# Kernel tuning notes

Hardware: AMD Instinct MI355X
Metric: run time of the kernel (lower is better)

## Reference

```python
import jax, jax.numpy as jnp
import numpy as np

B, L, S = 4, 1024, 1024
D_MODEL, H, DK = 1024, 16, 64  # d_model == H * DK required by the in-place writeback


def setup_inputs() -> dict:
    key = jax.random.key(0)
    ks = jax.random.split(key, 12)
    queries = jax.random.normal(ks[0], (B, L, D_MODEL), dtype=jnp.float32)
    keys = jax.random.normal(ks[1], (B, S, D_MODEL), dtype=jnp.float32)
    values = jax.random.normal(ks[2], (B, S, D_MODEL), dtype=jnp.float32)
    gate_scores = jax.random.uniform(ks[3], (B, H, DK, D_MODEL), dtype=jnp.float32)
    sc = 1.0 / np.sqrt(D_MODEL)
    W_q = jax.random.normal(ks[4], (H * DK, D_MODEL), dtype=jnp.float32) * sc
    b_q = jax.random.normal(ks[5], (H * DK,), dtype=jnp.float32) * 0.01
    W_k = jax.random.normal(ks[6], (H * DK, D_MODEL), dtype=jnp.float32) * sc
    b_k = jax.random.normal(ks[7], (H * DK,), dtype=jnp.float32) * 0.01
    W_v = jax.random.normal(ks[8], (H * DK, D_MODEL), dtype=jnp.float32) * sc
    b_v = jax.random.normal(ks[9], (H * DK,), dtype=jnp.float32) * 0.01
    W_o = jax.random.normal(ks[10], (D_MODEL, H * DK), dtype=jnp.float32) * sc
    b_o = jax.random.normal(ks[11], (D_MODEL,), dtype=jnp.float32) * 0.01
    return {"queries": queries, "keys": keys, "values": values,
            "gate_scores": gate_scores, "W_q": W_q, "b_q": b_q,
            "W_k": W_k, "b_k": b_k, "W_v": W_v, "b_v": b_v,
            "W_o": W_o, "b_o": b_o}


def reference(queries, keys, values, gate_scores, W_q, b_q, W_k, b_k, W_v, b_v, W_o, b_o):
    # Per-sample gated Q/K/V projection: W_x[b] = gate_scores[b] * W_x  (elementwise, [H,DK,Dm])
    # fused as a batched einsum instead of the per-sample Python loop.
    Wq = W_q.reshape(H, DK, D_MODEL)
    Wk = W_k.reshape(H, DK, D_MODEL)
    Wv = W_v.reshape(H, DK, D_MODEL)
    Q = jnp.einsum('blm,bhkm,hkm->blhk', queries, gate_scores, Wq) + b_q.reshape(H, DK)
    K = jnp.einsum('bsm,bhkm,hkm->bshk', keys, gate_scores, Wk) + b_k.reshape(H, DK)
    V = jnp.einsum('bsm,bhkm,hkm->bshk', values, gate_scores, Wv) + b_v.reshape(H, DK)
    # Full scaled dot-product attention (standard inner_attention)
    scale = 1.0 / jnp.sqrt(jnp.asarray(DK, Q.dtype))
    scores = jnp.einsum('blhk,bshk->bhls', Q, K) * scale
    attn = jax.nn.softmax(scores, axis=-1)
    out = jnp.einsum('bhls,bshk->blhk', attn, V).reshape(B, L, H * DK)
    out = out @ W_o.T + b_o
    return out, attn
```

## Files before the change

kernel.cpp:

```cpp
#include <hip/hip_runtime.h>
#include <math.h>

#define BB 4
#define LL 1024
#define SS 1024
#define DM 1024
#define HH 16
#define DKH 64
#define NH 1024
#define SM_SCALE 0.125f

typedef __attribute__((ext_vector_type(8))) short bf16x8;
typedef __attribute__((ext_vector_type(4))) float f32x4;
typedef unsigned short ushort_t;
typedef unsigned int uint_t;

#define MFMA16(a, b, c) __builtin_amdgcn_mfma_f32_16x16x32_bf16((a), (b), (c), 0, 0, 0)

__device__ __forceinline__ ushort_t f2b(float f) {
    union { float f; uint_t u; } x; x.f = f;
    uint_t r = x.u + 0x7fffu + ((x.u >> 16) & 1u);
    return (ushort_t)(r >> 16);
}

__device__ __forceinline__ float b2f(ushort_t v) {
    union { float f; uint_t u; } x; x.u = ((uint_t)v) << 16;
    return x.f;
}

__device__ __forceinline__ void gload_lds16(const void* g, void* l) {
    __builtin_amdgcn_global_load_lds(
        (const __attribute__((address_space(1))) unsigned int*)g,
        (__attribute__((address_space(3))) unsigned int*)l, 16, 0, 0);
}

__device__ __forceinline__ int xcd_swz(int lin, int nwg) {
    return (lin & 7) * (nwg >> 3) + (lin >> 3);
}

__device__ __forceinline__ void cvt8(const float* src, ushort_t* dst, const float* g2) {
    float4 a  = *(const float4*)(src);
    float4 b4 = *(const float4*)(src + 4);
    if (g2) {
        float4 ga = *(const float4*)(g2);
        float4 gb = *(const float4*)(g2 + 4);
        a.x *= ga.x; a.y *= ga.y; a.z *= ga.z; a.w *= ga.w;
        b4.x *= gb.x; b4.y *= gb.y; b4.z *= gb.z; b4.w *= gb.w;
    }
    uint4 o;
    o.x = f2b(a.x)  | ((uint_t)f2b(a.y)  << 16);
    o.y = f2b(a.z)  | ((uint_t)f2b(a.w)  << 16);
    o.z = f2b(b4.x) | ((uint_t)f2b(b4.y) << 16);
    o.w = f2b(b4.z) | ((uint_t)f2b(b4.w) << 16);
    *(uint4*)dst = o;
}

__global__ __launch_bounds__(256) void prep_kernel(
    const float* __restrict__ q, const float* __restrict__ k, const float* __restrict__ v,
    const float* __restrict__ gate,
    const float* __restrict__ Wq, const float* __restrict__ Wk, const float* __restrict__ Wv,
    const float* __restrict__ Wo,
    ushort_t* __restrict__ Xq, ushort_t* __restrict__ Xk, ushort_t* __restrict__ Xv,
    ushort_t* __restrict__ Gq, ushort_t* __restrict__ Gk, ushort_t* __restrict__ Gv,
    ushort_t* __restrict__ Wo2)
{
    const int XCH = 3 * 524288;
    const int GCH = 524288;
    const int WCH = 131072;
    for (int c = blockIdx.x * 256 + threadIdx.x; c < XCH + GCH + WCH; c += gridDim.x * 256) {
        if (c < XCH) {
            int r = c >> 19;
            int e = (c & 524287) * 8;
            cvt8((r == 0 ? q : r == 1 ? k : v) + e,
                 (r == 0 ? Xq : r == 1 ? Xk : Xv) + e, nullptr);
        } else if (c < XCH + GCH) {
            int e = (c - XCH) * 8;
            int nm = e & 1048575;
            const float* g2 = gate + e;
            cvt8(Wq + nm, Gq + e, g2);
            cvt8(Wk + nm, Gk + e, g2);
            cvt8(Wv + nm, Gv + e, g2);
        } else {
            int e = (c - XCH - GCH) * 8;
            cvt8(Wo + e, Wo2 + e, nullptr);
        }
    }
}

__global__ __launch_bounds__(256) void qkv_gemm(
    const ushort_t* __restrict__ Xq, const ushort_t* __restrict__ Gq, const float* __restrict__ bq,
    const ushort_t* __restrict__ Xk, const ushort_t* __restrict__ Gk, const float* __restrict__ bk,
    const ushort_t* __restrict__ Xv, const ushort_t* __restrict__ Gv, const float* __restrict__ bv,
    ushort_t* __restrict__ Qb, ushort_t* __restrict__ Kb, ushort_t* __restrict__ Vt,
    int mode)
{
    __shared__ ushort_t As[128 * 64];
    __shared__ ushort_t Bs[128 * 64];
    const int p  = xcd_swz(blockIdx.x, gridDim.x);
    const int g2 = p >> 6;
    const int r  = p & 63;
    int b, g;
    if (mode == 0)      { b = g2 / 3;  g = g2 % 3; }
    else if (mode == 1) { b = g2 >> 1; g = g2 & 1; }
    else                { b = g2;      g = 2;      }
    const size_t off = (size_t)b * 1048576;
    const ushort_t *A, *B; const float* bias; ushort_t* C; bool brow;
    if (g == 0)      { A = Xq + off; B = Gq + off; bias = bq; C = Qb + off; brow = false; }
    else if (g == 1) { A = Xk + off; B = Gk + off; bias = bk; C = Kb + off; brow = false; }
    else             { A = Gv + off; B = Xv + off; bias = bv; C = Vt + off; brow = true;  }

    const int bm = (r >> 3) * 128;
    const int bn = (r & 7) * 128;
    const int tid = threadIdx.x;
    const int lane = tid & 63;
    const int w = tid >> 6;
    const int wr = w >> 1, wc = w & 1;
    const int lr = lane & 15, lk = lane >> 4;

    f32x4 acc[4][4];
    #pragma unroll
    for (int i = 0; i < 4; ++i)
        #pragma unroll
        for (int j = 0; j < 4; ++j)
            acc[i][j] = (f32x4){0.f, 0.f, 0.f, 0.f};

    for (int k0 = 0; k0 < 1024; k0 += 64) {
        #pragma unroll
        for (int pp = 0; pp < 4; ++pp) {
            int f = pp * 256 + tid;
            int row = f >> 3, seg = f & 7;
            int kb2 = (seg * 8) ^ ((row & 7) * 8);
            gload_lds16(A + (size_t)(bm + row) * 1024 + k0 + kb2,
                        (char*)As + ((pp * 256 + (w << 6)) << 4));
            gload_lds16(B + (size_t)(bn + row) * 1024 + k0 + kb2,
                        (char*)Bs + ((pp * 256 + (w << 6)) << 4));
        }
        __syncthreads();
        #pragma unroll
        for (int kk = 0; kk < 2; ++kk) {
            bf16x8 af[4], bfr[4];
            #pragma unroll
            for (int i = 0; i < 4; ++i) {
                int row = wr * 64 + i * 16 + lr;
                af[i] = *(const bf16x8*)&As[row * 64 + ((lk * 8 + kk * 32) ^ ((row & 7) * 8))];
            }
            #pragma unroll
            for (int j = 0; j < 4; ++j) {
                int row = wc * 64 + j * 16 + lr;
                bfr[j] = *(const bf16x8*)&Bs[row * 64 + ((lk * 8 + kk * 32) ^ ((row & 7) * 8))];
            }
            #pragma unroll
            for (int i = 0; i < 4; ++i)
                #pragma unroll
                for (int j = 0; j < 4; ++j)
                    acc[i][j] = MFMA16(af[i], bfr[j], acc[i][j]);
        }
        __syncthreads();
    }

    #pragma unroll
    for (int i = 0; i < 4; ++i)
        #pragma unroll
        for (int j = 0; j < 4; ++j)
            #pragma unroll
            for (int rr = 0; rr < 4; ++rr) {
                int row = bm + wr * 64 + i * 16 + lk * 4 + rr;
                int col = bn + wc * 64 + j * 16 + lr;
                float vv = acc[i][j][rr] + bias[brow ? row : col];
                C[(size_t)row * 1024 + col] = f2b(vv);
            }
}

__global__ __launch_bounds__(256) void fused_attn_kernel(
    const ushort_t* __restrict__ Q, const ushort_t* __restrict__ Kmat,
    const ushort_t* __restrict__ Vt, float* __restrict__ attn,
    ushort_t* __restrict__ ctx)
{
    __shared__ ushort_t Ks[2][64 * 64];
    __shared__ ushort_t Vs[2][64 * 64];
    __shared__ ushort_t Ps[64 * 64];
    const int p  = xcd_swz(blockIdx.x, gridDim.x);
    const int bh = p >> 4;
    const int b  = bh >> 4;
    const int h  = bh & 15;
    const int r0 = (p & 15) * 64;
    const int tid = threadIdx.x, lane = tid & 63, w = tid >> 6;
    const int lr = lane & 15, lk = lane >> 4;

    bf16x8 aq[2];
    {
        const ushort_t* Qrow = Q + ((size_t)b * LL + r0 + w * 16 + lr) * NH + h * DKH;
        aq[0] = *(const bf16x8*)(Qrow + lk * 8);
        aq[1] = *(const bf16x8*)(Qrow + lk * 8 + 32);
    }
    const ushort_t* Kp = Kmat + (size_t)b * SS * NH + h * DKH;
    const ushort_t* Vp = Vt + ((size_t)b * NH + h * DKH) * SS;
    ushort_t* Psw = Ps + w * 1024;

    const int srow = tid >> 3;
    const int sseg = tid & 7;
    const int skb  = (sseg * 8) ^ ((srow & 7) * 8);
    const int skb1 = (sseg * 8) ^ (((srow + 32) & 7) * 8);

#define STAGE_K(t, buf)                                                          \
    do {                                                                         \
        gload_lds16(Kp + (size_t)((t) * 64 + srow) * NH + skb,                   \
                    (char*)(&Ks[buf][0]) + ((0 * 256 + (w << 6)) << 4));         \
        gload_lds16(Kp + (size_t)((t) * 64 + srow + 32) * NH + skb1,             \
                    (char*)(&Ks[buf][0]) + ((1 * 256 + (w << 6)) << 4));         \
    } while (0)
#define STAGE_V(t, buf)                                                          \
    do {                                                                         \
        gload_lds16(Vp + (size_t)srow * SS + (t) * 64 + skb,                     \
                    (char*)(&Vs[buf][0]) + ((0 * 256 + (w << 6)) << 4));         \
        gload_lds16(Vp + (size_t)(srow + 32) * SS + (t) * 64 + skb1,             \
                    (char*)(&Vs[buf][0]) + ((1 * 256 + (w << 6)) << 4));         \
    } while (0)

    float inv[4] = {0.f, 0.f, 0.f, 0.f};

    STAGE_K(0, 0);
    __syncthreads();
    for (int t = 0; t < 16; ++t) {
        const int cur = t & 1;
        if (t < 15) STAGE_K(t + 1, cur ^ 1);
        f32x4 acc[4];
        #pragma unroll
        for (int j = 0; j < 4; ++j) acc[j] = (f32x4){0.f, 0.f, 0.f, 0.f};
        #pragma unroll
        for (int kk = 0; kk < 2; ++kk)
            #pragma unroll
            for (int j = 0; j < 4; ++j) {
                int row = j * 16 + lr;
                bf16x8 bk2 = *(const bf16x8*)&Ks[cur][row * 64 + ((lk * 8 + kk * 32) ^ ((row & 7) * 8))];
                acc[j] = MFMA16(aq[kk], bk2, acc[j]);
            }
        #pragma unroll
        for (int rr = 0; rr < 4; ++rr)
            inv[rr] += __expf(SM_SCALE * acc[0][rr]) + __expf(SM_SCALE * acc[1][rr])
                     + __expf(SM_SCALE * acc[2][rr]) + __expf(SM_SCALE * acc[3][rr]);
        __syncthreads();
    }
    #pragma unroll
    for (int rr = 0; rr < 4; ++rr) {
        float s = inv[rr];
        s += __shfl_xor(s, 1);
        s += __shfl_xor(s, 2);
        s += __shfl_xor(s, 4);
        s += __shfl_xor(s, 8);
        inv[rr] = 1.0f / s;
    }

    f32x4 occ[4];
    #pragma unroll
    for (int j = 0; j < 4; ++j) occ[j] = (f32x4){0.f, 0.f, 0.f, 0.f};
    float* Ob = attn + (((size_t)b * HH + h) * LL + r0 + w * 16) * SS;
    const int erow = lane >> 3;
    const int eseg = lane & 7;

    STAGE_K(0, 0);
    STAGE_V(0, 0);
    __syncthreads();
    for (int t = 0; t < 16; ++t) {
        const int cur = t & 1;
        if (t < 15) { STAGE_K(t + 1, cur ^ 1); STAGE_V(t + 1, cur ^ 1); }
        f32x4 acc[4];
        #pragma unroll
        for (int j = 0; j < 4; ++j) acc[j] = (f32x4){0.f, 0.f, 0.f, 0.f};
        #pragma unroll
        for (int kk = 0; kk < 2; ++kk)
            #pragma unroll
            for (int j = 0; j < 4; ++j) {
                int row = j * 16 + lr;
                bf16x8 bk2 = *(const bf16x8*)&Ks[cur][row * 64 + ((lk * 8 + kk * 32) ^ ((row & 7) * 8))];
                acc[j] = MFMA16(aq[kk], bk2, acc[j]);
            }
        #pragma unroll
        for (int j = 0; j < 4; ++j)
            #pragma unroll
            for (int rr = 0; rr < 4; ++rr) {
                int ql = lk * 4 + rr;
                float pv = __expf(SM_SCALE * acc[j][rr]) * inv[rr];
                Psw[ql * 64 + ((j * 16 + lr) ^ ((ql & 7) * 8))] = f2b(pv);
            }
        #pragma unroll
        for (int kk = 0; kk < 2; ++kk) {
            bf16x8 pa = *(const bf16x8*)&Psw[lr * 64 + ((kk * 32 + lk * 8) ^ ((lr & 7) * 8))];
            #pragma unroll
            for (int j = 0; j < 4; ++j) {
                int row = j * 16 + lr;
                bf16x8 bv2 = *(const bf16x8*)&Vs[cur][row * 64 + ((kk * 32 + lk * 8) ^ ((row & 7) * 8))];
                occ[j] = MFMA16(pa, bv2, occ[j]);
            }
        }
        float* Obt = Ob + t * 64;
        #pragma unroll
        for (int hh = 0; hh < 2; ++hh) {
            int rl = erow + hh * 8;
            bf16x8 p8 = *(const bf16x8*)&Psw[rl * 64 + ((eseg * 8) ^ ((rl & 7) * 8))];
            float4 o0 = make_float4(b2f((ushort_t)p8[0]), b2f((ushort_t)p8[1]),
                                    b2f((ushort_t)p8[2]), b2f((ushort_t)p8[3]));
            float4 o1 = make_float4(b2f((ushort_t)p8[4]), b2f((ushort_t)p8[5]),
                                    b2f((ushort_t)p8[6]), b2f((ushort_t)p8[7]));
            *(float4*)(Obt + (size_t)rl * SS + eseg * 8) = o0;
            *(float4*)(Obt + (size_t)rl * SS + eseg * 8 + 4) = o1;
        }
        __syncthreads();
    }

    #pragma unroll
    for (int j = 0; j < 4; ++j)
        #pragma unroll
        for (int rr = 0; rr < 4; ++rr)
            ctx[((size_t)b * LL + r0 + w * 16 + lk * 4 + rr) * NH + h * DKH + j * 16 + lr]
                = f2b(occ[j][rr]);
#undef STAGE_K
#undef STAGE_V
}

__global__ __launch_bounds__(256) void out_gemm(
    const ushort_t* __restrict__ A, const ushort_t* __restrict__ B,
    const float* __restrict__ bias, float* __restrict__ C)
{
    __shared__ ushort_t As[128 * 64];
    __shared__ ushort_t Bs[64 * 64];
    const int p  = xcd_swz(blockIdx.x, gridDim.x);
    const int bm = (p >> 4) * 128;
    const int bn = (p & 15) * 64;
    const int tid = threadIdx.x;
    const int lane = tid & 63;
    const int w = tid >> 6;
    const int wr = w >> 1, wc = w & 1;
    const int lr = lane & 15, lk = lane >> 4;

    f32x4 acc[4][2];
    #pragma unroll
    for (int i = 0; i < 4; ++i)
        #pragma unroll
        for (int j = 0; j < 2; ++j)
            acc[i][j] = (f32x4){0.f, 0.f, 0.f, 0.f};

    for (int k0 = 0; k0 < 1024; k0 += 64) {
        #pragma unroll
        for (int pp = 0; pp < 4; ++pp) {
            int f = pp * 256 + tid;
            int row = f >> 3, seg = f & 7;
            int kb2 = (seg * 8) ^ ((row & 7) * 8);
            gload_lds16(A + (size_t)(bm + row) * 1024 + k0 + kb2,
                        (char*)As + ((pp * 256 + (w << 6)) << 4));
        }
        #pragma unroll
        for (int pp = 0; pp < 2; ++pp) {
            int f = pp * 256 + tid;
            int row = f >> 3, seg = f & 7;
            int kb2 = (seg * 8) ^ ((row & 7) * 8);
            gload_lds16(B + (size_t)(bn + row) * 1024 + k0 + kb2,
                        (char*)Bs + ((pp * 256 + (w << 6)) << 4));
        }
        __syncthreads();
        #pragma unroll
        for (int kk = 0; kk < 2; ++kk) {
            bf16x8 af[4], bfr[2];
            #pragma unroll
            for (int i = 0; i < 4; ++i) {
                int row = wr * 64 + i * 16 + lr;
                af[i] = *(const bf16x8*)&As[row * 64 + ((lk * 8 + kk * 32) ^ ((row & 7) * 8))];
            }
            #pragma unroll
            for (int j = 0; j < 2; ++j) {
                int row = wc * 32 + j * 16 + lr;
                bfr[j] = *(const bf16x8*)&Bs[row * 64 + ((lk * 8 + kk * 32) ^ ((row & 7) * 8))];
            }
            #pragma unroll
            for (int i = 0; i < 4; ++i)
                #pragma unroll
                for (int j = 0; j < 2; ++j)
                    acc[i][j] = MFMA16(af[i], bfr[j], acc[i][j]);
        }
        __syncthreads();
    }

    #pragma unroll
    for (int i = 0; i < 4; ++i)
        #pragma unroll
        for (int j = 0; j < 2; ++j)
            #pragma unroll
            for (int rr = 0; rr < 4; ++rr) {
                int row = bm + wr * 64 + i * 16 + lk * 4 + rr;
                int col = bn + wc * 32 + j * 16 + lr;
                C[(size_t)row * DM + col] = acc[i][j][rr] + bias[col];
            }
}

extern "C" void kernel_launch(void* const* d_in, const int* in_sizes, int n_in,
                              void* d_out, int out_size, void* d_ws, size_t ws_size,
                              hipStream_t stream)
{
    const float* queries = (const float*)d_in[0];
    const float* keys    = (const float*)d_in[1];
    const float* values  = (const float*)d_in[2];
    const float* gate    = (const float*)d_in[3];
    const float* W_q     = (const float*)d_in[4];
    const float* b_q     = (const float*)d_in[5];
    const float* W_k     = (const float*)d_in[6];
    const float* b_k     = (const float*)d_in[7];
    const float* W_v     = (const float*)d_in[8];
    const float* b_v     = (const float*)d_in[9];
    const float* W_o     = (const float*)d_in[10];
    const float* b_o     = (const float*)d_in[11];

    float* out  = (float*)d_out;
    float* attn = out + (size_t)BB * LL * DM;

    char* ws = (char*)d_ws;
    const size_t U = (size_t)8 << 20;
    ushort_t* Xq = (ushort_t*)(ws);
    ushort_t* Xk = (ushort_t*)(ws + 1 * U);
    ushort_t* Xv = (ushort_t*)(ws + 2 * U);
    ushort_t* Gq = (ushort_t*)(ws + 3 * U);
    ushort_t* Gk = (ushort_t*)(ws + 4 * U);
    ushort_t* Gv = (ushort_t*)(ws + 5 * U);
    ushort_t* Vt = (ushort_t*)(ws + 6 * U);
    const bool big = ws_size >= 9 * U + ((size_t)2 << 20);
    ushort_t *Qb, *Kb, *Wo2;
    if (big) { Qb = (ushort_t*)(ws + 7 * U); Kb = (ushort_t*)(ws + 8 * U); Wo2 = (ushort_t*)(ws + 9 * U); }
    else     { Qb = Xv; Kb = Gv; Wo2 = (ushort_t*)(ws + 7 * U); }
    ushort_t* ctx = Xq;

    dim3 blk(256, 1, 1);
    prep_kernel<<<2048, blk, 0, stream>>>(queries, keys, values, gate,
                                          W_q, W_k, W_v, W_o,
                                          Xq, Xk, Xv, Gq, Gk, Gv, Wo2);
    if (big) {
        qkv_gemm<<<768, blk, 0, stream>>>(Xq, Gq, b_q, Xk, Gk, b_k,
                                          Xv, Gv, b_v, Qb, Kb, Vt, 0);
    } else {
        qkv_gemm<<<256, blk, 0, stream>>>(Xq, Gq, b_q, Xk, Gk, b_k,
                                          Xv, Gv, b_v, Qb, Kb, Vt, 2);
        qkv_gemm<<<512, blk, 0, stream>>>(Xq, Gq, b_q, Xk, Gk, b_k,
                                          Xv, Gv, b_v, Qb, Kb, Vt, 1);
    }
    fused_attn_kernel<<<1024, blk, 0, stream>>>(Qb, Kb, Vt, attn, ctx);
    out_gemm<<<512, blk, 0, stream>>>(ctx, Wo2, b_o, out);
}
```

Measured before the change: 178.2 us.

## Cache unnormalized exp scores in registers to skip second QK^T pass

```diff
diff --git a/kernel.cpp b/kernel.cpp
--- a/kernel.cpp
+++ b/kernel.cpp
@@ -171,13 +171,12 @@
             }
 }
 
-__global__ __launch_bounds__(256) void fused_attn_kernel(
+__global__ __launch_bounds__(256, 2) void fused_attn_kernel(
     const ushort_t* __restrict__ Q, const ushort_t* __restrict__ Kmat,
     const ushort_t* __restrict__ Vt, float* __restrict__ attn,
     ushort_t* __restrict__ ctx)
 {
-    __shared__ ushort_t Ks[2][64 * 64];
-    __shared__ ushort_t Vs[2][64 * 64];
+    __shared__ ushort_t KVs[2][64 * 64];
     __shared__ ushort_t Ps[64 * 64];
     const int p  = xcd_swz(blockIdx.x, gridDim.x);
     const int bh = p >> 4;
@@ -205,22 +204,24 @@
 #define STAGE_K(t, buf)                                                          \
     do {                                                                         \
         gload_lds16(Kp + (size_t)((t) * 64 + srow) * NH + skb,                   \
-                    (char*)(&Ks[buf][0]) + ((0 * 256 + (w << 6)) << 4));         \
+                    (char*)(&KVs[buf][0]) + ((0 * 256 + (w << 6)) << 4));        \
         gload_lds16(Kp + (size_t)((t) * 64 + srow + 32) * NH + skb1,             \
-                    (char*)(&Ks[buf][0]) + ((1 * 256 + (w << 6)) << 4));         \
+                    (char*)(&KVs[buf][0]) + ((1 * 256 + (w << 6)) << 4));        \
     } while (0)
 #define STAGE_V(t, buf)                                                          \
     do {                                                                         \
         gload_lds16(Vp + (size_t)srow * SS + (t) * 64 + skb,                     \
-                    (char*)(&Vs[buf][0]) + ((0 * 256 + (w << 6)) << 4));         \
+                    (char*)(&KVs[buf][0]) + ((0 * 256 + (w << 6)) << 4));        \
         gload_lds16(Vp + (size_t)(srow + 32) * SS + (t) * 64 + skb1,             \
-                    (char*)(&Vs[buf][0]) + ((1 * 256 + (w << 6)) << 4));         \
+                    (char*)(&KVs[buf][0]) + ((1 * 256 + (w << 6)) << 4));        \
     } while (0)
 
     float inv[4] = {0.f, 0.f, 0.f, 0.f};
+    uint_t pk[16][8];
 
     STAGE_K(0, 0);
     __syncthreads();
+    #pragma unroll
     for (int t = 0; t < 16; ++t) {
         const int cur = t & 1;
         if (t < 15) STAGE_K(t + 1, cur ^ 1);
@@ -232,13 +233,19 @@
             #pragma unroll
             for (int j = 0; j < 4; ++j) {
                 int row = j * 16 + lr;
-                bf16x8 bk2 = *(const bf16x8*)&Ks[cur][row * 64 + ((lk * 8 + kk * 32) ^ ((row & 7) * 8))];
+                bf16x8 bk2 = *(const bf16x8*)&KVs[cur][row * 64 + ((lk * 8 + kk * 32) ^ ((row & 7) * 8))];
                 acc[j] = MFMA16(aq[kk], bk2, acc[j]);
             }
         #pragma unroll
-        for (int rr = 0; rr < 4; ++rr)
-            inv[rr] += __expf(SM_SCALE * acc[0][rr]) + __expf(SM_SCALE * acc[1][rr])
-                     + __expf(SM_SCALE * acc[2][rr]) + __expf(SM_SCALE * acc[3][rr]);
+        for (int j = 0; j < 4; ++j)
+            #pragma unroll
+            for (int hh = 0; hh < 2; ++hh) {
+                uint_t u0 = f2b(__expf(SM_SCALE * acc[j][2 * hh]));
+                uint_t u1 = f2b(__expf(SM_SCALE * acc[j][2 * hh + 1]));
+                pk[t][j * 2 + hh] = u0 | (u1 << 16);
+                inv[2 * hh]     += b2f((ushort_t)u0);
+                inv[2 * hh + 1] += b2f((ushort_t)u1);
+            }
         __syncthreads();
     }
     #pragma unroll
@@ -258,38 +265,27 @@
     const int erow = lane >> 3;
     const int eseg = lane & 7;
 
-    STAGE_K(0, 0);
     STAGE_V(0, 0);
     __syncthreads();
+    #pragma unroll
     for (int t = 0; t < 16; ++t) {
         const int cur = t & 1;
-        if (t < 15) { STAGE_K(t + 1, cur ^ 1); STAGE_V(t + 1, cur ^ 1); }
-        f32x4 acc[4];
-        #pragma unroll
-        for (int j = 0; j < 4; ++j) acc[j] = (f32x4){0.f, 0.f, 0.f, 0.f};
-        #pragma unroll
-        for (int kk = 0; kk < 2; ++kk)
+        if (t < 15) STAGE_V(t + 1, cur ^ 1);
+        #pragma unroll
+        for (int j = 0; j < 4; ++j)
+            #pragma unroll
+            for (int rr = 0; rr < 4; ++rr) {
+                int ql = lk * 4 + rr;
+                float ev = b2f((ushort_t)((pk[t][j * 2 + (rr >> 1)] >> ((rr & 1) * 16)) & 0xffffu));
+                Psw[ql * 64 + ((j * 16 + lr) ^ ((ql & 7) * 8))] = f2b(ev * inv[rr]);
+            }
+        #pragma unroll
+        for (int kk = 0; kk < 2; ++kk) {
+            bf16x8 pa = *(const bf16x8*)&Psw[lr * 64 + ((kk * 32 + lk * 8) ^ ((lr & 7) * 8))];
             #pragma unroll
             for (int j = 0; j < 4; ++j) {
                 int row = j * 16 + lr;
-                bf16x8 bk2 = *(const bf16x8*)&Ks[cur][row * 64 + ((lk * 8 + kk * 32) ^ ((row & 7) * 8))];
-                acc[j] = MFMA16(aq[kk], bk2, acc[j]);
-            }
-        #pragma unroll
-        for (int j = 0; j < 4; ++j)
-            #pragma unroll
-            for (int rr = 0; rr < 4; ++rr) {
-                int ql = lk * 4 + rr;
-                float pv = __expf(SM_SCALE * acc[j][rr]) * inv[rr];
-                Psw[ql * 64 + ((j * 16 + lr) ^ ((ql & 7) * 8))] = f2b(pv);
-            }
-        #pragma unroll
-        for (int kk = 0; kk < 2; ++kk) {
-            bf16x8 pa = *(const bf16x8*)&Psw[lr * 64 + ((kk * 32 + lk * 8) ^ ((lr & 7) * 8))];
-            #pragma unroll
-            for (int j = 0; j < 4; ++j) {
-                int row = j * 16 + lr;
-                bf16x8 bv2 = *(const bf16x8*)&Vs[cur][row * 64 + ((kk * 32 + lk * 8) ^ ((row & 7) * 8))];
+                bf16x8 bv2 = *(const bf16x8*)&KVs[cur][row * 64 + ((kk * 32 + lk * 8) ^ ((row & 7) * 8))];
                 occ[j] = MFMA16(pa, bv2, occ[j]);
             }
         }
@@ -298,12 +294,12 @@
         for (int hh = 0; hh < 2; ++hh) {
             int rl = erow + hh * 8;
             bf16x8 p8 = *(const bf16x8*)&Psw[rl * 64 + ((eseg * 8) ^ ((rl & 7) * 8))];
-            float4 o0 = make_float4(b2f((ushort_t)p8[0]), b2f((ushort_t)p8[1]),
-                                    b2f((ushort_t)p8[2]), b2f((ushort_t)p8[3]));
-            float4 o1 = make_float4(b2f((ushort_t)p8[4]), b2f((ushort_t)p8[5]),
-                                    b2f((ushort_t)p8[6]), b2f((ushort_t)p8[7]));
-            *(float4*)(Obt + (size_t)rl * SS + eseg * 8) = o0;
-            *(float4*)(Obt + (size_t)rl * SS + eseg * 8 + 4) = o1;
+            f32x4 o0 = {b2f((ushort_t)p8[0]), b2f((ushort_t)p8[1]),
+                        b2f((ushort_t)p8[2]), b2f((ushort_t)p8[3])};
+            f32x4 o1 = {b2f((ushort_t)p8[4]), b2f((ushort_t)p8[5]),
+                        b2f((ushort_t)p8[6]), b2f((ushort_t)p8[7])};
+            __builtin_nontemporal_store(o0, (f32x4*)(Obt + (size_t)rl * SS + eseg * 8));
+            __builtin_nontemporal_store(o1, (f32x4*)(Obt + (size_t)rl * SS + eseg * 8 + 4));
         }
         __syncthreads();
     }
```

After: 233.1 us. +30.8%, slower.

## Fold softmax scale into Q projection and use 128-row attention tiles with 512 threads

Applied to the files above, without the earlier changes.

```diff
diff --git a/kernel.cpp b/kernel.cpp
--- a/kernel.cpp
+++ b/kernel.cpp
@@ -8,7 +8,7 @@
 #define HH 16
 #define DKH 64
 #define NH 1024
-#define SM_SCALE 0.125f
+#define QK_ALPHA 0.1803368801f
 
 typedef __attribute__((ext_vector_type(8))) short bf16x8;
 typedef __attribute__((ext_vector_type(4))) float f32x4;
@@ -108,6 +108,7 @@
     if (g == 0)      { A = Xq + off; B = Gq + off; bias = bq; C = Qb + off; brow = false; }
     else if (g == 1) { A = Xk + off; B = Gk + off; bias = bk; C = Kb + off; brow = false; }
     else             { A = Gv + off; B = Xv + off; bias = bv; C = Vt + off; brow = true;  }
+    const float oscale = (g == 0) ? QK_ALPHA : 1.0f;
 
     const int bm = (r >> 3) * 128;
     const int bn = (r & 7) * 128;
@@ -166,24 +167,24 @@
             for (int rr = 0; rr < 4; ++rr) {
                 int row = bm + wr * 64 + i * 16 + lk * 4 + rr;
                 int col = bn + wc * 64 + j * 16 + lr;
-                float vv = acc[i][j][rr] + bias[brow ? row : col];
+                float vv = (acc[i][j][rr] + bias[brow ? row : col]) * oscale;
                 C[(size_t)row * 1024 + col] = f2b(vv);
             }
 }
 
-__global__ __launch_bounds__(256) void fused_attn_kernel(
+__global__ __launch_bounds__(512) void fused_attn_kernel(
     const ushort_t* __restrict__ Q, const ushort_t* __restrict__ Kmat,
     const ushort_t* __restrict__ Vt, float* __restrict__ attn,
     ushort_t* __restrict__ ctx)
 {
-    __shared__ ushort_t Ks[2][64 * 64];
-    __shared__ ushort_t Vs[2][64 * 64];
-    __shared__ ushort_t Ps[64 * 64];
+    __shared__ ushort_t K2[2][64 * 64];
+    __shared__ ushort_t V2[2][64 * 64];
+    __shared__ ushort_t Ps[8 * 1024];
     const int p  = xcd_swz(blockIdx.x, gridDim.x);
-    const int bh = p >> 4;
+    const int bh = p >> 3;
     const int b  = bh >> 4;
     const int h  = bh & 15;
-    const int r0 = (p & 15) * 64;
+    const int r0 = (p & 7) * 128;
     const int tid = threadIdx.x, lane = tid & 63, w = tid >> 6;
     const int lr = lane & 15, lk = lane >> 4;
 
@@ -200,22 +201,13 @@
     const int srow = tid >> 3;
     const int sseg = tid & 7;
     const int skb  = (sseg * 8) ^ ((srow & 7) * 8);
-    const int skb1 = (sseg * 8) ^ (((srow + 32) & 7) * 8);
-
-#define STAGE_K(t, buf)                                                          \
-    do {                                                                         \
-        gload_lds16(Kp + (size_t)((t) * 64 + srow) * NH + skb,                   \
-                    (char*)(&Ks[buf][0]) + ((0 * 256 + (w << 6)) << 4));         \
-        gload_lds16(Kp + (size_t)((t) * 64 + srow + 32) * NH + skb1,             \
-                    (char*)(&Ks[buf][0]) + ((1 * 256 + (w << 6)) << 4));         \
-    } while (0)
-#define STAGE_V(t, buf)                                                          \
-    do {                                                                         \
-        gload_lds16(Vp + (size_t)srow * SS + (t) * 64 + skb,                     \
-                    (char*)(&Vs[buf][0]) + ((0 * 256 + (w << 6)) << 4));         \
-        gload_lds16(Vp + (size_t)(srow + 32) * SS + (t) * 64 + skb1,             \
-                    (char*)(&Vs[buf][0]) + ((1 * 256 + (w << 6)) << 4));         \
-    } while (0)
+
+#define STAGE_K(t, buf)                                                         \
+    gload_lds16(Kp + (size_t)((t) * 64 + srow) * NH + skb,                      \
+                (char*)(&K2[buf][0]) + (w << 10))
+#define STAGE_V(t, buf)                                                         \
+    gload_lds16(Vp + (size_t)srow * SS + (t) * 64 + skb,                        \
+                (char*)(&V2[buf][0]) + (w << 10))
 
     float inv[4] = {0.f, 0.f, 0.f, 0.f};
 
@@ -232,13 +224,13 @@
             #pragma unroll
             for (int j = 0; j < 4; ++j) {
                 int row = j * 16 + lr;
-                bf16x8 bk2 = *(const bf16x8*)&Ks[cur][row * 64 + ((lk * 8 + kk * 32) ^ ((row & 7) * 8))];
+                bf16x8 bk2 = *(const bf16x8*)&K2[cur][row * 64 + ((lk * 8 + kk * 32) ^ ((row & 7) * 8))];
                 acc[j] = MFMA16(aq[kk], bk2, acc[j]);
             }
         #pragma unroll
         for (int rr = 0; rr < 4; ++rr)
-            inv[rr] += __expf(SM_SCALE * acc[0][rr]) + __expf(SM_SCALE * acc[1][rr])
-                     + __expf(SM_SCALE * acc[2][rr]) + __expf(SM_SCALE * acc[3][rr]);
+            inv[rr] += __builtin_amdgcn_exp2f(acc[0][rr]) + __builtin_amdgcn_exp2f(acc[1][rr])
+                     + __builtin_amdgcn_exp2f(acc[2][rr]) + __builtin_amdgcn_exp2f(acc[3][rr]);
         __syncthreads();
     }
     #pragma unroll
@@ -272,7 +264,7 @@
             #pragma unroll
             for (int j = 0; j < 4; ++j) {
                 int row = j * 16 + lr;
-                bf16x8 bk2 = *(const bf16x8*)&Ks[cur][row * 64 + ((lk * 8 + kk * 32) ^ ((row & 7) * 8))];
+                bf16x8 bk2 = *(const bf16x8*)&K2[cur][row * 64 + ((lk * 8 + kk * 32) ^ ((row & 7) * 8))];
                 acc[j] = MFMA16(aq[kk], bk2, acc[j]);
             }
         #pragma unroll
@@ -280,7 +272,7 @@
             #pragma unroll
             for (int rr = 0; rr < 4; ++rr) {
                 int ql = lk * 4 + rr;
-                float pv = __expf(SM_SCALE * acc[j][rr]) * inv[rr];
+                float pv = __builtin_amdgcn_exp2f(acc[j][rr]) * inv[rr];
                 Psw[ql * 64 + ((j * 16 + lr) ^ ((ql & 7) * 8))] = f2b(pv);
             }
         #pragma unroll
@@ -289,7 +281,7 @@
             #pragma unroll
             for (int j = 0; j < 4; ++j) {
                 int row = j * 16 + lr;
-                bf16x8 bv2 = *(const bf16x8*)&Vs[cur][row * 64 + ((kk * 32 + lk * 8) ^ ((row & 7) * 8))];
+                bf16x8 bv2 = *(const bf16x8*)&V2[cur][row * 64 + ((kk * 32 + lk * 8) ^ ((row & 7) * 8))];
                 occ[j] = MFMA16(pa, bv2, occ[j]);
             }
         }
@@ -440,6 +432,6 @@
         qkv_gemm<<<512, blk, 0, stream>>>(Xq, Gq, b_q, Xk, Gk, b_k,
                                           Xv, Gv, b_v, Qb, Kb, Vt, 1);
     }
-    fused_attn_kernel<<<1024, blk, 0, stream>>>(Qb, Kb, Vt, attn, ctx);
+    fused_attn_kernel<<<512, dim3(512, 1, 1), 0, stream>>>(Qb, Kb, Vt, attn, ctx);
     out_gemm<<<512, blk, 0, stream>>>(ctx, Wo2, b_o, out);
 }
```

Result: faster. 174.5 us (-2.1%).
